# Kernel optimization log

Hardware: AMD Instinct MI355X
Metric: run time of the kernel (lower is better)

Reference implementation:

```python
import jax, jax.numpy as jnp
import numpy as np

NEG_SLOPE = 0.2  # PyG GATConv default negative_slope


def setup_inputs() -> dict:
    key = jax.random.key(0)
    ks = jax.random.split(key, 10)
    B, N, E = 8, 10000, 160000
    Din, Dout = 128, 128
    x = jax.random.normal(ks[0], (B, N, Din), dtype=jnp.float32)
    src = jax.random.randint(ks[1], (E,), 0, N)
    dst = jax.random.randint(ks[2], (E,), 0, N)
    edge_index = jnp.stack([src, dst])  # [2, E]
    edge_attr = jax.random.uniform(ks[3], (E,), dtype=jnp.float32)
    lim = 1.0 / np.sqrt(Din)
    W = jax.random.uniform(ks[4], (Dout, Din), jnp.float32, -lim, lim)   # shared lin (src==dst)
    We = jax.random.uniform(ks[5], (Dout, 1), jnp.float32, -1.0, 1.0)    # lin_edge, edge_dim=1
    att_src = jax.random.normal(ks[6], (Dout,), jnp.float32) * 0.1
    att_dst = jax.random.normal(ks[7], (Dout,), jnp.float32) * 0.1
    att_edge = jax.random.normal(ks[8], (Dout,), jnp.float32) * 0.1
    bias = jnp.zeros((Dout,), jnp.float32)
    return {"x": x, "edge_index": edge_index, "edge_attr": edge_attr,
            "W": W, "We": We, "att_src": att_src, "att_dst": att_dst,
            "att_edge": att_edge, "bias": bias}


def reference(x, edge_index, edge_attr, W, We, att_src, att_dst, att_edge, bias):
    B, N, Din = x.shape
    src, dst = edge_index[0], edge_index[1]
    # --- add self loops with fill_value='mean' (mean of incoming edge_attr per node) ---
    deg = jax.ops.segment_sum(jnp.ones_like(edge_attr), dst, num_segments=N)
    loop_attr = jax.ops.segment_sum(edge_attr, dst, num_segments=N) / jnp.maximum(deg, 1.0)
    ar = jnp.arange(N, dtype=src.dtype)
    full_src = jnp.concatenate([src, ar])          # [E2]
    full_dst = jnp.concatenate([dst, ar])          # [E2]
    full_attr = jnp.concatenate([edge_attr, loop_attr])
    # edge features: Linear(1 -> Dout, no bias) == outer product; identical across batch
    e_feat = full_attr[:, None] * We[:, 0][None, :]        # [E2, Dout]
    alpha_e = e_feat @ att_edge                            # [E2]

    def single(xb):  # xb: [N, Din]
        h = xb @ W.T                                       # [N, Dout]
        a_src = h @ att_src                                # [N]
        a_dst = h @ att_dst                                # [N]
        a = a_src[full_src] + a_dst[full_dst] + alpha_e    # [E2]
        a = jax.nn.leaky_relu(a, NEG_SLOPE)
        # segment softmax over destination node
        a_max = jax.ops.segment_max(a, full_dst, num_segments=N)
        a_max = jnp.where(jnp.isfinite(a_max), a_max, 0.0)
        ex = jnp.exp(a - a_max[full_dst])
        s = jax.ops.segment_sum(ex, full_dst, num_segments=N)
        alpha = ex / (s[full_dst] + 1e-16)                 # [E2]
        out = jax.ops.segment_sum(alpha[:, None] * h[full_src], full_dst, num_segments=N)
        return out + bias, alpha

    x_out, attn = jax.vmap(single)(x)   # [B, N, Dout], [B, E2]
    return x_out, attn
```

## Files before the change

### kernel.cpp

```cpp
#include <hip/hip_runtime.h>
#include <hip/hip_bf16.h>
#include <hip/hip_fp16.h>

typedef short short8 __attribute__((ext_vector_type(8)));
typedef float floatx4 __attribute__((ext_vector_type(4)));

static constexpr int BATCH = 8;
static constexpr int NN    = 10000;
static constexpr int EE    = 160000;
static constexpr int EE2   = EE + NN;
static constexpr int DD    = 128;
static constexpr float SLOPE = 0.2f;
static constexpr long OUT_ELEMS = (long)BATCH * NN * DD;
static constexpr int EB = EE / 256;

__device__ inline float ldf(const void* p, long i, int f32) {
    return f32 ? ((const float*)p)[i]
               : __bfloat162float(((const __hip_bfloat16*)p)[i]);
}
__device__ inline int esrc(const int* ei, int e, int i64) { return i64 ? ei[2 * e] : ei[e]; }
__device__ inline int edst(const int* ei, int e, int i64) { return i64 ? ei[2 * (EE + e)] : ei[EE + e]; }
__device__ inline short bf16bits(float v) {
    __hip_bfloat16 b = __float2bfloat16(v);
    short s; __builtin_memcpy(&s, &b, 2); return s;
}
__device__ inline short f16bits(float v) {
    __half b = __float2half(v);
    short s; __builtin_memcpy(&s, &b, 2); return s;
}

__global__ __launch_bounds__(256) void k_detect(const unsigned short* __restrict__ xu,
                                                const int* __restrict__ ei,
                                                const void* __restrict__ We,
                                                const void* __restrict__ att_edge,
                                                int* __restrict__ flags,
                                                float* __restrict__ cout,
                                                int* __restrict__ deg,
                                                float* __restrict__ lsum) {
    int t = threadIdx.x;
    if (blockIdx.x > 0) {
        int idx = (blockIdx.x - 1) * 256 + t;
        if (idx < NN) { deg[idx] = 0; lsum[idx] = 0.f; }
        return;
    }
    __shared__ int cnt[2];
    __shared__ float red[256];
    if (t < 2) cnt[t] = 0;
    __syncthreads();
    int c1 = 0;
    for (int i = t; i < 32768; i += 256) {
        unsigned short u = xu[i];
        if ((u & 0x7F80u) == 0x7F80u) c1++;
    }
    int c2 = (ei[2 * t + 1] != 0) ? 1 : 0;
    if (c1) atomicAdd(&cnt[0], c1);
    if (c2) atomicAdd(&cnt[1], c2);
    __syncthreads();
    int f32 = (cnt[0] > 0);
    if (t == 0) { flags[0] = f32; flags[1] = (cnt[1] == 0); }
    red[t] = (t < DD) ? ldf(We, t, f32) * ldf(att_edge, t, f32) : 0.f;
    __syncthreads();
    for (int o = 128; o > 0; o >>= 1) {
        if (t < o) red[t] += red[t + o];
        __syncthreads();
    }
    if (t == 0) *cout = red[0];
}

__global__ __launch_bounds__(256) void k_deg(const int* __restrict__ ei,
                                             const void* __restrict__ attr,
                                             const void* __restrict__ W,
                                             const int* __restrict__ flags,
                                             int* __restrict__ deg, float* __restrict__ lsum,
                                             __hip_bfloat16* __restrict__ Wb) {
    int f32 = flags[0], i64 = flags[1];
    int bId = blockIdx.x, t = threadIdx.x;
    if (bId < EB) {
        int e = bId * 256 + t;
        int d = edst(ei, e, i64);
        atomicAdd(&deg[d], 1);
        atomicAdd(&lsum[d], ldf(attr, e, f32));
    } else {
        int idx = (bId - EB) * 512 + t * 2;
        if (f32) {
            float2 v = ((const float2*)W)[idx >> 1];
            Wb[idx]     = __float2bfloat16(v.x);
            Wb[idx + 1] = __float2bfloat16(v.y);
        } else {
            ((ushort2*)Wb)[idx >> 1] = ((const ushort2*)W)[idx >> 1];
        }
    }
}

template<int F32>
__device__ inline void load_a(const void* __restrict__ x, long row, int quad, short8 afr[4]) {
    if (F32) {
        const float* xr = (const float*)x + row * DD;
        #pragma unroll
        for (int kk = 0; kk < 4; kk++) {
            float4 f0 = *(const float4*)(xr + kk * 32 + quad * 8);
            float4 f1 = *(const float4*)(xr + kk * 32 + quad * 8 + 4);
            short8 a;
            a[0] = bf16bits(f0.x); a[1] = bf16bits(f0.y); a[2] = bf16bits(f0.z); a[3] = bf16bits(f0.w);
            a[4] = bf16bits(f1.x); a[5] = bf16bits(f1.y); a[6] = bf16bits(f1.z); a[7] = bf16bits(f1.w);
            afr[kk] = a;
        }
    } else {
        const short* xr = (const short*)x + row * DD;
        #pragma unroll
        for (int kk = 0; kk < 4; kk++)
            afr[kk] = *(const short8*)(xr + kk * 32 + quad * 8);
    }
}

__global__ __launch_bounds__(128) void k_gemm(const void* __restrict__ x,
                                              const __hip_bfloat16* __restrict__ Wb,
                                              const void* __restrict__ att_src,
                                              const void* __restrict__ att_dst,
                                              const int* __restrict__ flags,
                                              short* __restrict__ h,
                                              float* __restrict__ asrc_t, float* __restrict__ adst_t) {
    __shared__ float tile[2][16 * 132];
    int f32 = flags[0];
    int wave = threadIdx.x >> 6;
    int lane = threadIdx.x & 63;
    int l15  = lane & 15, quad = lane >> 4;
    long rows_base = (long)blockIdx.x * 32 + wave * 16;

    short8 afr[4];
    if (f32) load_a<1>(x, rows_base + l15, quad, afr);
    else     load_a<0>(x, rows_base + l15, quad, afr);

    const short* wr = (const short*)Wb;
    floatx4 acc[8];
    #pragma unroll
    for (int jt = 0; jt < 8; jt++) acc[jt] = (floatx4){0.f, 0.f, 0.f, 0.f};
    #pragma unroll
    for (int jt = 0; jt < 8; jt++) {
        #pragma unroll
        for (int kk = 0; kk < 4; kk++) {
            short8 bfr = *(const short8*)(wr + (jt * 16 + l15) * DD + kk * 32 + quad * 8);
            acc[jt] = __builtin_amdgcn_mfma_f32_16x16x32_bf16(afr[kk], bfr, acc[jt], 0, 0, 0);
        }
    }

    float asum[4] = {0.f, 0.f, 0.f, 0.f};
    float dsum[4] = {0.f, 0.f, 0.f, 0.f};
    #pragma unroll
    for (int jt = 0; jt < 8; jt++) {
        int col = jt * 16 + l15;
        float as = ldf(att_src, col, f32);
        float ad = ldf(att_dst, col, f32);
        #pragma unroll
        for (int r = 0; r < 4; r++) {
            asum[r] += acc[jt][r] * as;
            dsum[r] += acc[jt][r] * ad;
        }
    }
    #pragma unroll
    for (int r = 0; r < 4; r++) {
        float a = asum[r], d = dsum[r];
        #pragma unroll
        for (int o = 1; o < 16; o <<= 1) { a += __shfl_xor(a, o, 64); d += __shfl_xor(d, o, 64); }
        if (l15 == 0) {
            long row = rows_base + quad * 4 + r;
            int b = (int)(row / NN), n = (int)(row - (long)b * NN);
            asrc_t[n * 8 + b] = a;
            adst_t[n * 8 + b] = d;
        }
    }

    float* tl = &tile[wave][0];
    #pragma unroll
    for (int jt = 0; jt < 8; jt++)
        #pragma unroll
        for (int r = 0; r < 4; r++)
            tl[(quad * 4 + r) * 132 + jt * 16 + l15] = acc[jt][r];
    #pragma unroll
    for (int it = 0; it < 4; it++) {
        int row = it * 4 + quad;
        float4 f0 = *(const float4*)&tl[row * 132 + l15 * 8];
        float4 f1 = *(const float4*)&tl[row * 132 + l15 * 8 + 4];
        short8 o;
        o[0] = f16bits(f0.x); o[1] = f16bits(f0.y); o[2] = f16bits(f0.z); o[3] = f16bits(f0.w);
        o[4] = f16bits(f1.x); o[5] = f16bits(f1.y); o[6] = f16bits(f1.z); o[7] = f16bits(f1.w);
        *(short8*)(h + (rows_base + row) * DD + l15 * 8) = o;
    }
}

__global__ __launch_bounds__(1024) void k_scan(const int* __restrict__ deg, int* __restrict__ offs) {
    __shared__ int part[1024];
    int t = threadIdx.x;
    const int PER = (NN + 1023) / 1024;
    int base = t * PER;
    int s = 0;
    for (int i = 0; i < PER; i++) { int idx = base + i; if (idx < NN) s += deg[idx]; }
    part[t] = s;
    __syncthreads();
    for (int o = 1; o < 1024; o <<= 1) {
        int v = (t >= o) ? part[t - o] : 0;
        __syncthreads();
        part[t] += v;
        __syncthreads();
    }
    int run = (t == 0) ? 0 : part[t - 1];
    for (int i = 0; i < PER; i++) {
        int idx = base + i;
        if (idx < NN) { offs[idx] = run; run += deg[idx]; }
    }
    if (t == 1023) offs[NN] = run;
}

__global__ __launch_bounds__(256) void k_fill(const int* __restrict__ ei,
                                              const void* __restrict__ attr,
                                              const int* __restrict__ flags,
                                              const float* __restrict__ cptr,
                                              int* __restrict__ offs,
                                              int2* __restrict__ edges) {
    int f32 = flags[0], i64 = flags[1];
    int e = blockIdx.x * 256 + threadIdx.x;
    float c = *cptr;
    if (e < EE) {
        int d = edst(ei, e, i64);
        int s = esrc(ei, e, i64);
        float at = ldf(attr, e, f32);
        int p = atomicAdd(&offs[d], 1);
        edges[p] = make_int2(s, __float_as_int(c * at));
    }
}

__global__ __launch_bounds__(256, 4) void k_agg(const int2* __restrict__ edges,
                                                const float* __restrict__ asrc_t,
                                                const float* __restrict__ adst_t,
                                                const __half* __restrict__ h,
                                                const int* __restrict__ deg,
                                                const float* __restrict__ lsum,
                                                const int* __restrict__ offs,
                                                const float* __restrict__ cptr,
                                                const void* __restrict__ bias,
                                                const int* __restrict__ flags,
                                                float* __restrict__ invT,
                                                void* __restrict__ outbuf) {
    int f32 = flags[0];
    int tid = threadIdx.x;
    int lane = tid & 63;
    int g   = lane >> 4;
    int c16 = tid & 15;
    int wv  = tid >> 6;
    int laneBase = lane & 48;
    int b = blockIdx.x & 7;
    int n = (blockIdx.x >> 3) * 16 + wv * 4 + g;

    float c   = *cptr;
    int dg    = deg[n];
    int off   = offs[n] - dg;
    int cnt   = dg + 1;
    int np    = (cnt + 1) >> 1;
    float atcS = c * (lsum[n] / fmaxf((float)dg, 1.0f));
    float an  = adst_t[n * 8 + b];

    const int2* em = edges + off;
    const __half* hb = h + (long)b * NN * DD;

    float acc[8];
    #pragma unroll
    for (int j = 0; j < 8; j++) acc[j] = 0.f;
    float ssum = 0.f;

#define LOADM(K, DST)                                                       \
    {   int _idx = (K) * 16 + c16;                                          \
        if (_idx < dg) DST = em[_idx];                                      \
        else { DST.x = n; DST.y = __float_as_int(atcS); }                   \
    }

#define MSTEP(PD)                                                           \
    if (((PD) & 7) == 0) {                                                  \
        int _kc = ((PD) >> 3) + 1;                                          \
        int2 _t; LOADM(_kc, _t);                                            \
        if (_kc & 1) mvB = _t; else mvA = _t;                               \
    }

#define DISSUE(PD, HV0, HV1, AR0, AR1, AT0, AT1)                            \
    {   int _j0 = ((PD) << 1) & 15;                                         \
        int _mx = (((PD) >> 3) & 1) ? mvB.x : mvA.x;                        \
        int _my = (((PD) >> 3) & 1) ? mvB.y : mvA.y;                        \
        int _s0 = __shfl(_mx, laneBase | _j0);                              \
        int _s1 = __shfl(_mx, laneBase | (_j0 + 1));                        \
        AT0 = __int_as_float(__shfl(_my, laneBase | _j0));                  \
        AT1 = __int_as_float(__shfl(_my, laneBase | (_j0 + 1)));            \
        AR0 = asrc_t[_s0 * 8 + b];                                          \
        AR1 = asrc_t[_s1 * 8 + b];                                          \
        HV0 = *(const uint4*)(hb + (long)_s0 * DD + c16 * 8);               \
        HV1 = *(const uint4*)(hb + (long)_s1 * DD + c16 * 8);               \
    }

#define CONSUME(P, HV0, HV1, AR0, AR1, AT0, AT1)                            \
    {   float _a0 = AR0 + an + AT0;                                         \
        _a0 = fmaxf(_a0, SLOPE * _a0);                                      \
        float _e0 = __expf(_a0);                                            \
        ssum += _e0;                                                        \
        const __half* _h0 = (const __half*)&HV0;                            \
        _Pragma("unroll")                                                   \
        for (int _j = 0; _j < 8; _j++)                                      \
            acc[_j] += _e0 * __half2float(_h0[_j]);                         \
        if (2 * (P) + 1 < cnt) {                                            \
            float _a1 = AR1 + an + AT1;                                     \
            _a1 = fmaxf(_a1, SLOPE * _a1);                                  \
            float _e1 = __expf(_a1);                                        \
            ssum += _e1;                                                    \
            const __half* _h1 = (const __half*)&HV1;                        \
            _Pragma("unroll")                                               \
            for (int _j = 0; _j < 8; _j++)                                  \
                acc[_j] += _e1 * __half2float(_h1[_j]);                     \
        }                                                                   \
    }

    int2 mvA, mvB;
    LOADM(0, mvA);
    LOADM(1, mvB);
    uint4 hA0, hA1, hB0, hB1, hC0, hC1;
    float arA0, arA1, atA0, atA1;
    float arB0, arB1, atB0, atB1;
    float arC0, arC1, atC0, atC1;
    DISSUE(0, hA0, hA1, arA0, arA1, atA0, atA1);
    DISSUE(1, hB0, hB1, arB0, arB1, atB0, atB1);

    for (int p = 0; p < np; p += 3) {
        MSTEP(p + 2);
        DISSUE(p + 2, hC0, hC1, arC0, arC1, atC0, atC1);
        CONSUME(p, hA0, hA1, arA0, arA1, atA0, atA1);
        if (p + 1 >= np) break;
        MSTEP(p + 3);
        DISSUE(p + 3, hA0, hA1, arA0, arA1, atA0, atA1);
        CONSUME(p + 1, hB0, hB1, arB0, arB1, atB0, atB1);
        if (p + 2 >= np) break;
        MSTEP(p + 4);
        DISSUE(p + 4, hB0, hB1, arB0, arB1, atB0, atB1);
        CONSUME(p + 2, hC0, hC1, arC0, arC1, atC0, atC1);
    }
#undef LOADM
#undef MSTEP
#undef DISSUE
#undef CONSUME

    float inv = 1.0f / (ssum + 1e-16f);
    if (c16 == 0) invT[n * 8 + b] = inv;
    #pragma unroll
    for (int j = 0; j < 8; j++) acc[j] = acc[j] * inv + ldf(bias, c16 * 8 + j, f32);

    long row = (long)b * NN + n;
    if (f32) {
        float4 lo = {acc[0], acc[1], acc[2], acc[3]};
        float4 hi = {acc[4], acc[5], acc[6], acc[7]};
        float4* orow = (float4*)((float*)outbuf + row * DD);
        orow[c16 * 2]     = lo;
        orow[c16 * 2 + 1] = hi;
    } else {
        short8 o;
        #pragma unroll
        for (int j = 0; j < 8; j++) o[j] = bf16bits(acc[j]);
        ((short8*)((__hip_bfloat16*)outbuf + row * DD))[c16] = o;
    }
}

__global__ __launch_bounds__(256) void k_attn(const int* __restrict__ ei,
                                              const void* __restrict__ attr,
                                              const float* __restrict__ asrc_t,
                                              const float* __restrict__ adst_t,
                                              const int* __restrict__ deg,
                                              const float* __restrict__ lsum,
                                              const float* __restrict__ cptr,
                                              const float* __restrict__ invT,
                                              const int* __restrict__ flags,
                                              void* __restrict__ outbuf) {
    int f32 = flags[0], i64 = flags[1];
    int e2 = blockIdx.x * 256 + threadIdx.x;
    if (e2 >= EE2) return;
    float c = *cptr;
    int s, d; float at;
    if (e2 < EE) {
        s = esrc(ei, e2, i64);
        d = edst(ei, e2, i64);
        at = ldf(attr, e2, f32);
    } else {
        int nn = e2 - EE;
        s = nn; d = nn;
        at = lsum[nn] / fmaxf((float)deg[nn], 1.0f);
    }
    float4 as0 = *(const float4*)(asrc_t + (long)s * 8);
    float4 as1 = *(const float4*)(asrc_t + (long)s * 8 + 4);
    float4 ad0 = *(const float4*)(adst_t + (long)d * 8);
    float4 ad1 = *(const float4*)(adst_t + (long)d * 8 + 4);
    float4 iv0 = *(const float4*)(invT   + (long)d * 8);
    float4 iv1 = *(const float4*)(invT   + (long)d * 8 + 4);
    float asv[8] = {as0.x, as0.y, as0.z, as0.w, as1.x, as1.y, as1.z, as1.w};
    float adv[8] = {ad0.x, ad0.y, ad0.z, ad0.w, ad1.x, ad1.y, ad1.z, ad1.w};
    float ivv[8] = {iv0.x, iv0.y, iv0.z, iv0.w, iv1.x, iv1.y, iv1.z, iv1.w};
    float ca = c * at;
    #pragma unroll
    for (int b = 0; b < BATCH; b++) {
        float a = asv[b] + adv[b] + ca;
        a = (a > 0.f) ? a : SLOPE * a;
        float al = __expf(a) * ivv[b];
        long gidx = OUT_ELEMS + (long)b * EE2 + e2;
        if (f32) ((float*)outbuf)[gidx] = al;
        else     ((__hip_bfloat16*)outbuf)[gidx] = __float2bfloat16(al);
    }
}

extern "C" void kernel_launch(void* const* d_in, const int* in_sizes, int n_in,
                              void* d_out, int out_size, void* d_ws, size_t ws_size,
                              hipStream_t stream) {
    const void* x        = d_in[0];
    const int*  ei       = (const int*)d_in[1];
    const void* attr     = d_in[2];
    const void* W        = d_in[3];
    const void* We       = d_in[4];
    const void* att_src  = d_in[5];
    const void* att_dst  = d_in[6];
    const void* att_edge = d_in[7];
    const void* bias     = d_in[8];

    char* ws = (char*)d_ws;
    size_t off = 0;
    auto alloc = [&](size_t bytes) { size_t o = off; off = (off + bytes + 255) & ~(size_t)255; return o; };
    short* h             = (short*)(ws + alloc((size_t)BATCH * NN * DD * 2));
    float* asrc_t        = (float*)(ws + alloc((size_t)NN * 8 * 4));
    float* adst_t        = (float*)(ws + alloc((size_t)NN * 8 * 4));
    float* invT          = (float*)(ws + alloc((size_t)NN * 8 * 4));
    int*   deg           = (int*)  (ws + alloc((size_t)NN * 4));
    float* lsum          = (float*)(ws + alloc((size_t)NN * 4));
    int*   offs          = (int*)  (ws + alloc((size_t)(NN + 1) * 4));
    int2*  edges         = (int2*) (ws + alloc((size_t)EE * 8));
    __hip_bfloat16* Wb   = (__hip_bfloat16*)(ws + alloc((size_t)DD * DD * 2));
    float* cscal         = (float*)(ws + alloc(256));
    int*   flags         = (int*)  (ws + alloc(256));

    k_detect<<<41, 256, 0, stream>>>((const unsigned short*)x, ei, We, att_edge,
                                     flags, cscal, deg, lsum);
    k_deg   <<<EB + 32, 256, 0, stream>>>(ei, attr, W, flags, deg, lsum, Wb);
    k_gemm  <<<(BATCH * NN) / 32, 128, 0, stream>>>(x, Wb, att_src, att_dst, flags,
                                                    h, asrc_t, adst_t);
    k_scan  <<<1, 1024, 0, stream>>>(deg, offs);
    k_fill  <<<EB, 256, 0, stream>>>(ei, attr, flags, cscal, offs, edges);
    k_agg   <<<(BATCH * NN) / 16, 256, 0, stream>>>(edges, asrc_t, adst_t, (const __half*)h,
                                                    deg, lsum, offs, cscal, bias, flags,
                                                    invT, d_out);
    k_attn  <<<(EE2 + 255) / 256, 256, 0, stream>>>(ei, attr, asrc_t, adst_t, deg, lsum,
                                                    cscal, invT, flags, d_out);
}
```

Measured before the change: 249.3 us.

## Sort nodes by degree for aggregation and deepen gather prefetch pipeline

The scan kernel now also builds a counting-sort permutation of nodes by descending in-degree, and the aggregation kernel processes nodes in that order, so the four nodes sharing a wave have similar edge counts and finish together. The aggregation loop's software pipeline is deepened from three to five in-flight edge-pair buffers to hide more gather latency. The cost is extra serial work in the single-block scan kernel, an indirection load per node, scattered output rows, and higher register pressure from the larger prefetch buffers.

Result: slower. 258.4 us (+3.7%).

```diff
diff --git a/kernel.cpp b/kernel.cpp
--- a/kernel.cpp
+++ b/kernel.cpp
@@ -188,8 +188,11 @@
     }
 }
 
-__global__ __launch_bounds__(1024) void k_scan(const int* __restrict__ deg, int* __restrict__ offs) {
+__global__ __launch_bounds__(1024) void k_scan(const int* __restrict__ deg,
+                                               int* __restrict__ offs,
+                                               int* __restrict__ perm) {
     __shared__ int part[1024];
+    __shared__ int hist[512];
     int t = threadIdx.x;
     const int PER = (NN + 1023) / 1024;
     int base = t * PER;
@@ -209,6 +212,26 @@
         if (idx < NN) { offs[idx] = run; run += deg[idx]; }
     }
     if (t == 1023) offs[NN] = run;
+
+    if (t < 512) hist[t] = 0;
+    __syncthreads();
+    for (int i = t; i < NN; i += 1024) atomicAdd(&hist[min(deg[i], 511)], 1);
+    __syncthreads();
+    if (t < 512) part[t] = hist[511 - t];
+    __syncthreads();
+    for (int o = 1; o < 512; o <<= 1) {
+        int v = (t >= o && t < 512) ? part[t - o] : 0;
+        __syncthreads();
+        if (t < 512) part[t] += v;
+        __syncthreads();
+    }
+    if (t < 512) hist[t] = (t == 511) ? 0 : part[510 - t];
+    __syncthreads();
+    for (int i = t; i < NN; i += 1024) {
+        int bn = min(deg[i], 511);
+        int p = atomicAdd(&hist[bn], 1);
+        perm[p] = i;
+    }
 }
 
 __global__ __launch_bounds__(256) void k_fill(const int* __restrict__ ei,
@@ -229,7 +252,8 @@
     }
 }
 
-__global__ __launch_bounds__(256, 4) void k_agg(const int2* __restrict__ edges,
+__global__ __launch_bounds__(256, 4) void k_agg(const int* __restrict__ perm,
+                                                const int2* __restrict__ edges,
                                                 const float* __restrict__ asrc_t,
                                                 const float* __restrict__ adst_t,
                                                 const __half* __restrict__ h,
@@ -249,7 +273,8 @@
     int wv  = tid >> 6;
     int laneBase = lane & 48;
     int b = blockIdx.x & 7;
-    int n = (blockIdx.x >> 3) * 16 + wv * 4 + g;
+    int slot = (blockIdx.x >> 3) * 16 + wv * 4 + g;
+    int n = perm[slot];
 
     float c   = *cptr;
     int dg    = deg[n];
@@ -318,25 +343,39 @@
     int2 mvA, mvB;
     LOADM(0, mvA);
     LOADM(1, mvB);
-    uint4 hA0, hA1, hB0, hB1, hC0, hC1;
-    float arA0, arA1, atA0, atA1;
-    float arB0, arB1, atB0, atB1;
-    float arC0, arC1, atC0, atC1;
+    uint4 z4 = {0, 0, 0, 0};
+    uint4 hA0 = z4, hA1 = z4, hB0 = z4, hB1 = z4, hC0 = z4, hC1 = z4,
+          hD0 = z4, hD1 = z4, hE0 = z4, hE1 = z4;
+    float arA0 = 0.f, arA1 = 0.f, atA0 = 0.f, atA1 = 0.f;
+    float arB0 = 0.f, arB1 = 0.f, atB0 = 0.f, atB1 = 0.f;
+    float arC0 = 0.f, arC1 = 0.f, atC0 = 0.f, atC1 = 0.f;
+    float arD0 = 0.f, arD1 = 0.f, atD0 = 0.f, atD1 = 0.f;
+    float arE0 = 0.f, arE1 = 0.f, atE0 = 0.f, atE1 = 0.f;
     DISSUE(0, hA0, hA1, arA0, arA1, atA0, atA1);
-    DISSUE(1, hB0, hB1, arB0, arB1, atB0, atB1);
-
-    for (int p = 0; p < np; p += 3) {
-        MSTEP(p + 2);
-        DISSUE(p + 2, hC0, hC1, arC0, arC1, atC0, atC1);
+    if (1 < np) DISSUE(1, hB0, hB1, arB0, arB1, atB0, atB1);
+    if (2 < np) DISSUE(2, hC0, hC1, arC0, arC1, atC0, atC1);
+    if (3 < np) DISSUE(3, hD0, hD1, arD0, arD1, atD0, atD1);
+
+    for (int p = 0; p < np; p += 5) {
+        MSTEP(p + 4);
+        if (p + 4 < np) DISSUE(p + 4, hE0, hE1, arE0, arE1, atE0, atE1);
         CONSUME(p, hA0, hA1, arA0, arA1, atA0, atA1);
         if (p + 1 >= np) break;
-        MSTEP(p + 3);
-        DISSUE(p + 3, hA0, hA1, arA0, arA1, atA0, atA1);
+        MSTEP(p + 5);
+        if (p + 5 < np) DISSUE(p + 5, hA0, hA1, arA0, arA1, atA0, atA1);
         CONSUME(p + 1, hB0, hB1, arB0, arB1, atB0, atB1);
         if (p + 2 >= np) break;
-        MSTEP(p + 4);
-        DISSUE(p + 4, hB0, hB1, arB0, arB1, atB0, atB1);
+        MSTEP(p + 6);
+        if (p + 6 < np) DISSUE(p + 6, hB0, hB1, arB0, arB1, atB0, atB1);
         CONSUME(p + 2, hC0, hC1, arC0, arC1, atC0, atC1);
+        if (p + 3 >= np) break;
+        MSTEP(p + 7);
+        if (p + 7 < np) DISSUE(p + 7, hC0, hC1, arC0, arC1, atC0, atC1);
+        CONSUME(p + 3, hD0, hD1, arD0, arD1, atD0, atD1);
+        if (p + 4 >= np) break;
+        MSTEP(p + 8);
+        if (p + 8 < np) DISSUE(p + 8, hD0, hD1, arD0, arD1, atD0, atD1);
+        CONSUME(p + 4, hE0, hE1, arE0, arE1, atE0, atE1);
     }
 #undef LOADM
 #undef MSTEP
@@ -431,6 +470,7 @@
     int*   deg           = (int*)  (ws + alloc((size_t)NN * 4));
     float* lsum          = (float*)(ws + alloc((size_t)NN * 4));
     int*   offs          = (int*)  (ws + alloc((size_t)(NN + 1) * 4));
+    int*   permv         = (int*)  (ws + alloc((size_t)NN * 4));
     int2*  edges         = (int2*) (ws + alloc((size_t)EE * 8));
     __hip_bfloat16* Wb   = (__hip_bfloat16*)(ws + alloc((size_t)DD * DD * 2));
     float* cscal         = (float*)(ws + alloc(256));
@@ -441,9 +481,9 @@
     k_deg   <<<EB + 32, 256, 0, stream>>>(ei, attr, W, flags, deg, lsum, Wb);
     k_gemm  <<<(BATCH * NN) / 32, 128, 0, stream>>>(x, Wb, att_src, att_dst, flags,
                                                     h, asrc_t, adst_t);
-    k_scan  <<<1, 1024, 0, stream>>>(deg, offs);
+    k_scan  <<<1, 1024, 0, stream>>>(deg, offs, permv);
     k_fill  <<<EB, 256, 0, stream>>>(ei, attr, flags, cscal, offs, edges);
-    k_agg   <<<(BATCH * NN) / 16, 256, 0, stream>>>(edges, asrc_t, adst_t, (const __half*)h,
+    k_agg   <<<(BATCH * NN) / 16, 256, 0, stream>>>(permv, edges, asrc_t, adst_t, (const __half*)h,
                                                     deg, lsum, offs, cscal, bias, flags,
                                                     invT, d_out);
     k_attn  <<<(EE2 + 255) / 256, 256, 0, stream>>>(ei, attr, asrc_t, adst_t, deg, lsum,
```
